# Optimization experiments

Measured on AMD Instinct MI355X. Metric: run time of the kernel, lower is better.

## Reference

```python
import jax, jax.numpy as jnp
import numpy as np

V, D, DU, H = 50000, 256, 1024, 128
TEMP = 0.01

def time_cosine_emb(t, d_model):
    half = d_model // 2
    div_term = jnp.exp(jnp.arange(half, dtype=jnp.float32) * (-np.log(10000.0) / half))
    scaled = t[..., None] * div_term  # (B, L, half)
    return jnp.concatenate([jnp.sin(scaled), jnp.cos(scaled)], axis=-1)

def setup_inputs() -> dict:
    key = jax.random.key(0)
    ks = jax.random.split(key, 12)
    B, L = 64, 2048
    q_seq = jax.random.randint(ks[0], (B, L), 0, V)
    r_seq = jax.random.randint(ks[1], (B, L), 0, 3)
    t_seq = jax.random.uniform(ks[2], (B, L), dtype=jnp.float32) * 1000.0
    mask = jnp.ones((B, L), dtype=jnp.float32)
    q_tab = jax.random.normal(ks[3], (V, D), dtype=jnp.float32) * 0.02
    q_tab = q_tab.at[0].set(0.0)  # padding_idx=0
    r_tab = jax.random.normal(ks[4], (3, D), dtype=jnp.float32) * 0.02
    r_tab = r_tab.at[0].set(0.0)  # padding_idx=0
    virtual_node = jax.random.normal(ks[5], (1, D), dtype=jnp.float32)
    Ws1 = jax.random.normal(ks[6], (H, 2 * D), dtype=jnp.float32) * (1.0 / np.sqrt(2 * D))
    bs1 = jnp.zeros((H,), dtype=jnp.float32)
    Ws2 = jax.random.normal(ks[7], (1, H), dtype=jnp.float32) * (1.0 / np.sqrt(H))
    bs2 = jnp.zeros((1,), dtype=jnp.float32)
    Wa = jax.random.normal(ks[8], (DU, D), dtype=jnp.float32) * (1.0 / np.sqrt(D))
    ba = jnp.zeros((DU,), dtype=jnp.float32)
    return {"q_seq": q_seq, "r_seq": r_seq, "t_seq": t_seq, "mask": mask,
            "q_tab": q_tab, "r_tab": r_tab, "virtual_node": virtual_node,
            "Ws1": Ws1, "bs1": bs1, "Ws2": Ws2, "bs2": bs2, "Wa": Wa, "ba": ba}

def reference(q_seq, r_seq, t_seq, mask, q_tab, r_tab, virtual_node, Ws1, bs1, Ws2, bs2, Wa, ba):
    B, L = q_seq.shape
    d_model = q_tab.shape[1]
    # embedding gathers + trig time embedding
    h_events = q_tab[q_seq] + r_tab[r_seq] + time_cosine_emb(t_seq, d_model)  # (B,L,D)
    h_virtual = jnp.broadcast_to(virtual_node[None, :, :], (B, L, d_model))
    pair = jnp.concatenate([h_events, h_virtual], axis=-1)  # (B,L,2D)
    # struct_head: Linear -> LeakyReLU(0.2) -> Linear
    hdn = jax.nn.leaky_relu(jnp.einsum('bld,hd->blh', pair, Ws1) + bs1, 0.2)
    logits = jnp.einsum('blh,oh->blo', hdn, Ws2) + bs2  # (B,L,1)
    A_hat = jax.nn.sigmoid(logits / TEMP) * mask[..., None]
    # aggregator: Linear -> LeakyReLU(0.2)
    h_trans = jax.nn.leaky_relu(jnp.einsum('bld,ud->blu', h_events, Wa) + ba, 0.2)  # (B,L,DU)
    u_i = jnp.sum(h_trans * A_hat, axis=1)  # (B,DU)
    return (u_i, jnp.squeeze(A_hat, -1))
```

## Files before the change

kernel.cpp:

```cpp
#include <hip/hip_runtime.h>

typedef unsigned short ushort_t;
typedef unsigned int uint_t;

typedef short bf16x8 __attribute__((ext_vector_type(8)));
typedef float f32x4 __attribute__((ext_vector_type(4)));

#define MFMA16(a, b, c) __builtin_amdgcn_mfma_f32_16x16x32_bf16(a, b, c, 0, 0, 0)

__device__ __forceinline__ ushort_t f2bf(float f) {
    uint_t u = __float_as_uint(f);
    u += 0x7fffu + ((u >> 16) & 1u);
    return (ushort_t)(u >> 16);
}
__device__ __forceinline__ float bf2f(ushort_t h) {
    return __uint_as_float(((uint_t)h) << 16);
}

__device__ __forceinline__ void async16(const ushort_t* g, ushort_t* l) {
    __builtin_amdgcn_global_load_lds(
        (const __attribute__((address_space(1))) uint_t*)g,
        (__attribute__((address_space(3))) uint_t*)l, 16, 0, 0);
}

__global__ void k_prep(const float* __restrict__ Ws1, const float* __restrict__ bs1,
                       const float* __restrict__ virt, const float* __restrict__ Wa,
                       float* __restrict__ consth, ushort_t* __restrict__ wa_b,
                       ushort_t* __restrict__ ws1h, ushort_t* __restrict__ ws1l) {
    int b = blockIdx.x;
    if (b == 0) {
        int h = threadIdx.x;
        if (h < 128) {
            const float* row = Ws1 + h * 512 + 256;
            float s = bs1[h];
            for (int d = 0; d < 256; ++d) s += row[d] * virt[d];
            consth[h] = s;
        }
        return;
    }
    const float* src;
    int src_stride, tid;
    ushort_t *dhi, *dlo;
    if (b <= 128) {
        tid = (b - 1) * 256 + threadIdx.x;
        src = Wa; src_stride = 256; dhi = wa_b; dlo = nullptr;
    } else {
        tid = (b - 129) * 256 + threadIdx.x;
        src = Ws1; src_stride = 512; dhi = ws1h; dlo = ws1l;
    }
    int pl = tid & 15, kc = (tid >> 4) & 31, pt = tid >> 9;
    int row = pt * 16 + pl;
    const float* s = src + (size_t)row * src_stride + kc * 8;
    ushort_t hs[8], ls[8];
#pragma unroll
    for (int j = 0; j < 8; ++j) {
        float v = s[j];
        ushort_t h = f2bf(v);
        hs[j] = h;
        ls[j] = f2bf(v - bf2f(h));
    }
    uint4 hv;
    hv.x = hs[0] | ((uint_t)hs[1] << 16); hv.y = hs[2] | ((uint_t)hs[3] << 16);
    hv.z = hs[4] | ((uint_t)hs[5] << 16); hv.w = hs[6] | ((uint_t)hs[7] << 16);
    *(uint4*)(dhi + (size_t)tid * 8) = hv;
    if (dlo) {
        uint4 lv;
        lv.x = ls[0] | ((uint_t)ls[1] << 16); lv.y = ls[2] | ((uint_t)ls[3] << 16);
        lv.z = ls[4] | ((uint_t)ls[5] << 16); lv.w = ls[6] | ((uint_t)ls[7] << 16);
        *(uint4*)(dlo + (size_t)tid * 8) = lv;
    }
}

__global__ __launch_bounds__(256, 1) void k_embed_struct(
    const int* __restrict__ q_seq, const int* __restrict__ r_seq,
    const float* __restrict__ t_seq, const float* __restrict__ q_tab,
    const float* __restrict__ r_tab,
    const ushort_t* __restrict__ ws1h, const ushort_t* __restrict__ ws1l,
    const float* __restrict__ consth, const float* __restrict__ Ws2,
    const float* __restrict__ bs2, const float* __restrict__ mask,
    ushort_t* __restrict__ h_hi, float* __restrict__ out_ahat) {
    __shared__ ushort_t sQ[33280];
    __shared__ ushort_t sAhi[16384];
    __shared__ ushort_t sAlo[16384];
    __shared__ float sdiv[128];
    __shared__ float sLogit[64];
    int tid = threadIdx.x;
    if (tid < 128) sdiv[tid] = __expf((float)tid * -0.07195578415606394f);
    if (tid < 64) sLogit[tid] = 0.0f;
    int w = tid >> 6, lane = tid & 63;
    int pl = lane & 15, kq = lane >> 4;
    int nl = pl;
    int p0 = blockIdx.x * 64;
    int p = p0 + w * 16 + pl;
    int qv = q_seq[p0 + w * 16 + (lane & 15)];
    int rr = r_seq[p];
    float tt = t_seq[p];
#pragma unroll
    for (int i = 0; i < 16; ++i) {
        int row = __shfl(qv, i, 64);
        async16((const ushort_t*)(q_tab + (size_t)row * 256) + lane * 8,
                sQ + (w * 16 + i) * 520);
    }
    __syncthreads();
    const char* myrow = (const char*)sQ + (w * 16 + pl) * 1040;
    const float* rrow = r_tab + (size_t)rr * 256;
#pragma unroll
    for (int it = 0; it < 8; ++it) {
        int kc = it * 4 + kq;
        int k0 = kc * 8;
        float4 qa = *(const float4*)(myrow + kc * 32);
        float4 qb = *(const float4*)(myrow + kc * 32 + 16);
        float4 ra = *(const float4*)(rrow + kc * 8);
        float4 rb = *(const float4*)(rrow + kc * 8 + 4);
        float v[8] = {qa.x + ra.x, qa.y + ra.y, qa.z + ra.z, qa.w + ra.w,
                      qb.x + rb.x, qb.y + rb.y, qb.z + rb.z, qb.w + rb.w};
        bool iscos = (kc >= 16);
#pragma unroll
        for (int j = 0; j < 8; ++j) {
            float ang = tt * sdiv[(k0 + j) & 127];
            v[j] += iscos ? __cosf(ang) : __sinf(ang);
        }
        ushort_t hs[8], ls[8];
#pragma unroll
        for (int j = 0; j < 8; ++j) {
            ushort_t h = f2bf(v[j]);
            hs[j] = h;
            ls[j] = f2bf(v[j] - bf2f(h));
        }
        uint4 hv, lv;
        hv.x = hs[0] | ((uint_t)hs[1] << 16); hv.y = hs[2] | ((uint_t)hs[3] << 16);
        hv.z = hs[4] | ((uint_t)hs[5] << 16); hv.w = hs[6] | ((uint_t)hs[7] << 16);
        lv.x = ls[0] | ((uint_t)ls[1] << 16); lv.y = ls[2] | ((uint_t)ls[3] << 16);
        lv.z = ls[4] | ((uint_t)ls[5] << 16); lv.w = ls[6] | ((uint_t)ls[7] << 16);
        *(uint4*)(h_hi + ((size_t)((blockIdx.x * 4 + w) * 32 + kc) * 16 + pl) * 8) = hv;
        int loff = ((w * 32 + kc) * 16 + pl) * 8;
        *(uint4*)(sAhi + loff) = hv;
        *(uint4*)(sAlo + loff) = lv;
    }
    __syncthreads();
    f32x4 acc[4][2];
    f32x4 z4 = {0.f, 0.f, 0.f, 0.f};
#pragma unroll
    for (int mt = 0; mt < 4; ++mt)
#pragma unroll
        for (int nt = 0; nt < 2; ++nt) acc[mt][nt] = z4;
    bf16x8 bhi[2], blo[2], nbhi[2], nblo[2];
#pragma unroll
    for (int nt = 0; nt < 2; ++nt) {
        int off = (((w * 2 + nt) * 32 + kq) * 16 + nl) * 8;
        bhi[nt] = *(const bf16x8*)(ws1h + off);
        blo[nt] = *(const bf16x8*)(ws1l + off);
    }
#pragma unroll 1
    for (int ks = 0; ks < 8; ++ks) {
        if (ks < 7) {
#pragma unroll
            for (int nt = 0; nt < 2; ++nt) {
                int off = (((w * 2 + nt) * 32 + (ks + 1) * 4 + kq) * 16 + nl) * 8;
                nbhi[nt] = *(const bf16x8*)(ws1h + off);
                nblo[nt] = *(const bf16x8*)(ws1l + off);
            }
        }
        bf16x8 ahi[4], alo[4];
#pragma unroll
        for (int mt = 0; mt < 4; ++mt) {
            int off = ((mt * 32 + ks * 4 + kq) * 16 + nl) * 8;
            ahi[mt] = *(const bf16x8*)&sAhi[off];
            alo[mt] = *(const bf16x8*)&sAlo[off];
        }
#pragma unroll
        for (int mt = 0; mt < 4; ++mt)
#pragma unroll
            for (int nt = 0; nt < 2; ++nt) {
                acc[mt][nt] = MFMA16(ahi[mt], bhi[nt], acc[mt][nt]);
                acc[mt][nt] = MFMA16(alo[mt], bhi[nt], acc[mt][nt]);
                acc[mt][nt] = MFMA16(ahi[mt], blo[nt], acc[mt][nt]);
            }
#pragma unroll
        for (int nt = 0; nt < 2; ++nt) { bhi[nt] = nbhi[nt]; blo[nt] = nblo[nt]; }
    }
    float ps[4][4];
#pragma unroll
    for (int mt = 0; mt < 4; ++mt)
#pragma unroll
        for (int r = 0; r < 4; ++r) ps[mt][r] = 0.f;
#pragma unroll
    for (int nt = 0; nt < 2; ++nt) {
        int ng = w * 32 + nt * 16 + nl;
        float chv = consth[ng], w2 = Ws2[ng];
#pragma unroll
        for (int mt = 0; mt < 4; ++mt)
#pragma unroll
            for (int r = 0; r < 4; ++r) {
                float v = acc[mt][nt][r] + chv;
                v = v > 0.f ? v : 0.2f * v;
                ps[mt][r] += v * w2;
            }
    }
#pragma unroll
    for (int mt = 0; mt < 4; ++mt)
#pragma unroll
        for (int r = 0; r < 4; ++r) {
            float x = ps[mt][r];
            x += __shfl_xor(x, 1, 64);
            x += __shfl_xor(x, 2, 64);
            x += __shfl_xor(x, 4, 64);
            x += __shfl_xor(x, 8, 64);
            ps[mt][r] = x;
        }
    if (nl == 0) {
#pragma unroll
        for (int mt = 0; mt < 4; ++mt)
#pragma unroll
            for (int r = 0; r < 4; ++r)
                atomicAdd(&sLogit[mt * 16 + kq * 4 + r], ps[mt][r]);
    }
    __syncthreads();
    if (tid < 64) {
        int pp = p0 + tid;
        float lg = sLogit[tid] + bs2[0];
        float y = lg * 100.0f;
        y = fminf(fmaxf(y, -60.f), 60.f);
        float a = 1.0f / (1.0f + expf(-y));
        out_ahat[pp] = a * mask[pp];
    }
}

__global__ __launch_bounds__(256, 2) void k_agg(
    const ushort_t* __restrict__ h_hi, const ushort_t* __restrict__ wa_blk,
    const float* __restrict__ ba, const float* __restrict__ ahat,
    float* __restrict__ u_i) {
    __shared__ ushort_t sB[32768];
    __shared__ float sAh[128];
    int tid = threadIdx.x;
    int w = tid >> 6, lane = tid & 63, nl = lane & 15, kq = lane >> 4;
    int p0 = blockIdx.x * 128, bidx = p0 >> 11;
    if (tid < 128) sAh[tid] = ahat[p0 + tid];
    int mh = w & 1, nh = w >> 1;
    bf16x8 afr[4][8];
    const ushort_t* gA = h_hi + (size_t)(p0 >> 4) * 4096;
#pragma unroll
    for (int mt = 0; mt < 4; ++mt) {
        const ushort_t* base = gA + (size_t)(mh * 4 + mt) * 4096;
#pragma unroll
        for (int ks = 0; ks < 8; ++ks)
            afr[mt][ks] = *(const bf16x8*)(base + ks * 512 + lane * 8);
    }
#pragma unroll 1
    for (int nch = 0; nch < 8; ++nch) {
        const ushort_t* gB = wa_blk + (size_t)nch * 32768;
#pragma unroll
        for (int i = 0; i < 16; ++i)
            async16(gB + (w * 16 + i) * 512 + lane * 8, sB + (w * 16 + i) * 512);
        __syncthreads();
        f32x4 acc[4][4];
        f32x4 z4 = {0.f, 0.f, 0.f, 0.f};
#pragma unroll
        for (int mt = 0; mt < 4; ++mt)
#pragma unroll
            for (int nt = 0; nt < 4; ++nt) acc[mt][nt] = z4;
#pragma unroll
        for (int ks = 0; ks < 8; ++ks) {
            bf16x8 bfr[4];
#pragma unroll
            for (int nt = 0; nt < 4; ++nt) {
                int ntl = nh * 4 + nt;
                bfr[nt] = *(const bf16x8*)&sB[ntl * 4096 + ks * 512 + lane * 8];
            }
#pragma unroll
            for (int mt = 0; mt < 4; ++mt)
#pragma unroll
                for (int nt = 0; nt < 4; ++nt)
                    acc[mt][nt] = MFMA16(afr[mt][ks], bfr[nt], acc[mt][nt]);
        }
        int n0 = nch * 128;
#pragma unroll
        for (int nt = 0; nt < 4; ++nt) {
            int ng = n0 + nh * 64 + nt * 16 + nl;
            float ban = ba[ng];
            float s = 0.f;
#pragma unroll
            for (int mt = 0; mt < 4; ++mt)
#pragma unroll
                for (int r = 0; r < 4; ++r) {
                    float v = acc[mt][nt][r] + ban;
                    v = v > 0.f ? v : 0.2f * v;
                    int ml = mh * 64 + mt * 16 + kq * 4 + r;
                    s += v * sAh[ml];
                }
            s += __shfl_xor(s, 16, 64);
            s += __shfl_xor(s, 32, 64);
            if (kq == 0) atomicAdd(&u_i[bidx * 1024 + ng], s);
        }
        __syncthreads();
    }
}

extern "C" void kernel_launch(void* const* d_in, const int* in_sizes, int n_in,
                              void* d_out, int out_size, void* d_ws, size_t ws_size,
                              hipStream_t stream) {
    const int* q_seq = (const int*)d_in[0];
    const int* r_seq = (const int*)d_in[1];
    const float* t_seq = (const float*)d_in[2];
    const float* mask = (const float*)d_in[3];
    const float* q_tab = (const float*)d_in[4];
    const float* r_tab = (const float*)d_in[5];
    const float* virt = (const float*)d_in[6];
    const float* Ws1 = (const float*)d_in[7];
    const float* bs1 = (const float*)d_in[8];
    const float* Ws2 = (const float*)d_in[9];
    const float* bs2 = (const float*)d_in[10];
    const float* Wa = (const float*)d_in[11];
    const float* ba = (const float*)d_in[12];
    float* out = (float*)d_out;

    ushort_t* h_hi = (ushort_t*)d_ws;
    ushort_t* wa_b = h_hi + 33554432;
    ushort_t* ws1h = wa_b + 262144;
    ushort_t* ws1l = ws1h + 32768;
    float* ch = (float*)(ws1l + 32768);

    hipMemsetAsync(out, 0, 65536 * sizeof(float), stream);
    hipLaunchKernelGGL(k_prep, dim3(145), dim3(256), 0, stream,
                       Ws1, bs1, virt, Wa, ch, wa_b, ws1h, ws1l);
    hipLaunchKernelGGL(k_embed_struct, dim3(2048), dim3(256), 0, stream,
                       q_seq, r_seq, t_seq, q_tab, r_tab, ws1h, ws1l, ch, Ws2, bs2,
                       mask, h_hi, out + 65536);
    hipLaunchKernelGGL(k_agg, dim3(1024), dim3(256), 0, stream,
                       h_hi, wa_b, ba, out + 65536, out);
}
```

Measured before the change: 273.2 us.

## Alias embed LDS buffers for 2 blocks/CU and double-buffer Wa in aggregator

```diff
diff --git a/kernel.cpp b/kernel.cpp
--- a/kernel.cpp
+++ b/kernel.cpp
@@ -71,7 +71,7 @@
     }
 }
 
-__global__ __launch_bounds__(256, 1) void k_embed_struct(
+__global__ __launch_bounds__(256, 2) void k_embed_struct(
     const int* __restrict__ q_seq, const int* __restrict__ r_seq,
     const float* __restrict__ t_seq, const float* __restrict__ q_tab,
     const float* __restrict__ r_tab,
@@ -79,11 +79,12 @@
     const float* __restrict__ consth, const float* __restrict__ Ws2,
     const float* __restrict__ bs2, const float* __restrict__ mask,
     ushort_t* __restrict__ h_hi, float* __restrict__ out_ahat) {
-    __shared__ ushort_t sQ[33280];
-    __shared__ ushort_t sAhi[16384];
-    __shared__ ushort_t sAlo[16384];
+    __shared__ __align__(16) char region[66560];
     __shared__ float sdiv[128];
     __shared__ float sLogit[64];
+    ushort_t* sQ = (ushort_t*)region;
+    ushort_t* sAhi = (ushort_t*)region;
+    ushort_t* sAlo = (ushort_t*)(region + 32768);
     int tid = threadIdx.x;
     if (tid < 128) sdiv[tid] = __expf((float)tid * -0.07195578415606394f);
     if (tid < 64) sLogit[tid] = 0.0f;
@@ -92,7 +93,7 @@
     int nl = pl;
     int p0 = blockIdx.x * 64;
     int p = p0 + w * 16 + pl;
-    int qv = q_seq[p0 + w * 16 + (lane & 15)];
+    int qv = q_seq[p0 + w * 16 + pl];
     int rr = r_seq[p];
     float tt = t_seq[p];
 #pragma unroll
@@ -102,6 +103,7 @@
                 sQ + (w * 16 + i) * 520);
     }
     __syncthreads();
+    uint4 hvA[8], lvA[8];
     const char* myrow = (const char*)sQ + (w * 16 + pl) * 1040;
     const float* rrow = r_tab + (size_t)rr * 256;
 #pragma unroll
@@ -132,10 +134,16 @@
         hv.z = hs[4] | ((uint_t)hs[5] << 16); hv.w = hs[6] | ((uint_t)hs[7] << 16);
         lv.x = ls[0] | ((uint_t)ls[1] << 16); lv.y = ls[2] | ((uint_t)ls[3] << 16);
         lv.z = ls[4] | ((uint_t)ls[5] << 16); lv.w = ls[6] | ((uint_t)ls[7] << 16);
+        hvA[it] = hv; lvA[it] = lv;
         *(uint4*)(h_hi + ((size_t)((blockIdx.x * 4 + w) * 32 + kc) * 16 + pl) * 8) = hv;
+    }
+    __syncthreads();
+#pragma unroll
+    for (int it = 0; it < 8; ++it) {
+        int kc = it * 4 + kq;
         int loff = ((w * 32 + kc) * 16 + pl) * 8;
-        *(uint4*)(sAhi + loff) = hv;
-        *(uint4*)(sAlo + loff) = lv;
+        *(uint4*)(sAhi + loff) = hvA[it];
+        *(uint4*)(sAlo + loff) = lvA[it];
     }
     __syncthreads();
     f32x4 acc[4][2];
@@ -230,7 +238,7 @@
     const ushort_t* __restrict__ h_hi, const ushort_t* __restrict__ wa_blk,
     const float* __restrict__ ba, const float* __restrict__ ahat,
     float* __restrict__ u_i) {
-    __shared__ ushort_t sB[32768];
+    __shared__ ushort_t sB[2][16384];
     __shared__ float sAh[128];
     int tid = threadIdx.x;
     int w = tid >> 6, lane = tid & 63, nl = lane & 15, kq = lane >> 4;
@@ -246,33 +254,57 @@
         for (int ks = 0; ks < 8; ++ks)
             afr[mt][ks] = *(const bf16x8*)(base + ks * 512 + lane * 8);
     }
+#define STAGE_HALF(buf, nch_, kh_)                                              \
+    {                                                                           \
+        int t0 = w * 2;                                                         \
+        _Pragma("unroll")                                                       \
+        for (int tt = 0; tt < 2; ++tt) {                                        \
+            int t = t0 + tt;                                                    \
+            const ushort_t* src =                                               \
+                wa_blk + (size_t)((nch_) * 8 + t) * 4096 + (kh_) * 2048;        \
+            _Pragma("unroll")                                                   \
+            for (int c = 0; c < 4; ++c)                                         \
+                async16(src + c * 512 + lane * 8, &sB[buf][t * 2048 + c * 512]);\
+        }                                                                       \
+    }
+    f32x4 acc[4][4];
+    f32x4 z4 = {0.f, 0.f, 0.f, 0.f};
+#pragma unroll
+    for (int mt = 0; mt < 4; ++mt)
+#pragma unroll
+        for (int nt = 0; nt < 4; ++nt) acc[mt][nt] = z4;
+    STAGE_HALF(0, 0, 0);
+    __syncthreads();
 #pragma unroll 1
     for (int nch = 0; nch < 8; ++nch) {
-        const ushort_t* gB = wa_blk + (size_t)nch * 32768;
-#pragma unroll
-        for (int i = 0; i < 16; ++i)
-            async16(gB + (w * 16 + i) * 512 + lane * 8, sB + (w * 16 + i) * 512);
+        STAGE_HALF(1, nch, 1);
+#pragma unroll
+        for (int ksl = 0; ksl < 4; ++ksl) {
+            bf16x8 bfr[4];
+#pragma unroll
+            for (int nt = 0; nt < 4; ++nt)
+                bfr[nt] = *(const bf16x8*)&sB[0][(nh * 4 + nt) * 2048 + (ksl * 4 + kq) * 128 + nl * 8];
+#pragma unroll
+            for (int mt = 0; mt < 4; ++mt)
+#pragma unroll
+                for (int nt = 0; nt < 4; ++nt)
+                    acc[mt][nt] = MFMA16(afr[mt][ksl], bfr[nt], acc[mt][nt]);
+        }
         __syncthreads();
-        f32x4 acc[4][4];
-        f32x4 z4 = {0.f, 0.f, 0.f, 0.f};
-#pragma unroll
-        for (int mt = 0; mt < 4; ++mt)
-#pragma unroll
-            for (int nt = 0; nt < 4; ++nt) acc[mt][nt] = z4;
-#pragma unroll
-        for (int ks = 0; ks < 8; ++ks) {
+        if (nch < 7) STAGE_HALF(0, nch + 1, 0);
+#pragma unroll
+        for (int ksl = 0; ksl < 4; ++ksl) {
             bf16x8 bfr[4];
 #pragma unroll
-            for (int nt = 0; nt < 4; ++nt) {
-                int ntl = nh * 4 + nt;
-                bfr[nt] = *(const bf16x8*)&sB[ntl * 4096 + ks * 512 + lane * 8];
-            }
+            for (int nt = 0; nt < 4; ++nt)
+                bfr[nt] = *(const bf16x8*)&sB[1][(nh * 4 + nt) * 2048 + (ksl * 4 + kq) * 128 + nl * 8];
 #pragma unroll
             for (int mt = 0; mt < 4; ++mt)
 #pragma unroll
                 for (int nt = 0; nt < 4; ++nt)
-                    acc[mt][nt] = MFMA16(afr[mt][ks], bfr[nt], acc[mt][nt]);
-        }
+                    acc[mt][nt] = MFMA16(afr[mt][4 + ksl], bfr[nt], acc[mt][nt]);
+        }
+        __syncthreads();
         int n0 = nch * 128;
 #pragma unroll
         for (int nt = 0; nt < 4; ++nt) {
@@ -287,13 +319,14 @@
                     v = v > 0.f ? v : 0.2f * v;
                     int ml = mh * 64 + mt * 16 + kq * 4 + r;
                     s += v * sAh[ml];
+                    acc[mt][nt][r] = 0.f;
                 }
             s += __shfl_xor(s, 16, 64);
             s += __shfl_xor(s, 32, 64);
             if (kq == 0) atomicAdd(&u_i[bidx * 1024 + ng], s);
         }
-        __syncthreads();
-    }
+    }
+#undef STAGE_HALF
 }
 
 extern "C" void kernel_launch(void* const* d_in, const int* in_sizes, int n_in,
```

New measurement: 259.3 us. -5.1%, faster.
